# Performance work log

Hardware: AMD Instinct MI355X
Metric: run time of the kernel (lower is better)

The kernel has to match this reference:

```python
import jax, jax.numpy as jnp
import numpy as np

GRID_SIZE = 5
SPLINE_ORDER = 3
KH, KW = 3, 3
STRIDE, PAD, DIL = 1, 1, 1


def make_grid(in_features, dtype=jnp.float32):
    # uniform grid over [-1, 1], extended by spline_order on each side
    h = 2.0 / GRID_SIZE
    g = jnp.arange(-SPLINE_ORDER, GRID_SIZE + SPLINE_ORDER + 1, dtype=dtype) * h - 1.0
    return jnp.broadcast_to(g, (in_features, g.shape[0]))  # (in, G)


def b_splines(x, grid):
    # x: (N, in); grid: (in, G). Cox-de Boor recursion.
    xg = x[..., None]  # (N, in, 1)
    bases = ((xg >= grid[:, :-1]) & (xg < grid[:, 1:])).astype(x.dtype)  # (N, in, G-1)
    for k in range(1, SPLINE_ORDER + 1):
        left = (xg - grid[:, : -(k + 1)]) / (grid[:, k:-1] - grid[:, : -(k + 1)])
        right = (grid[:, k + 1:] - xg) / (grid[:, k + 1:] - grid[:, 1:-k])
        bases = left * bases[..., :-1] + right * bases[..., 1:]
    return bases  # (N, in, grid_size + spline_order)


def setup_inputs() -> dict:
    key = jax.random.key(0)
    k1, k2, k3, k4 = jax.random.split(key, 4)
    B, C, H, W = 4, 64, 64, 64
    out_ch = 128
    patch_dim = C * KH * KW  # 576
    nbasis = GRID_SIZE + SPLINE_ORDER  # 8
    x = jax.random.normal(k1, (B, C, H, W), dtype=jnp.float32)
    base_weight = jax.random.normal(k2, (out_ch, patch_dim), dtype=jnp.float32) * 0.05
    spline_weight = jax.random.normal(k3, (out_ch, patch_dim, nbasis), dtype=jnp.float32) * 0.05
    spline_scaler = jax.random.normal(k4, (out_ch, patch_dim), dtype=jnp.float32) * 0.1 + 1.0
    return {"x": x, "base_weight": base_weight, "spline_weight": spline_weight, "spline_scaler": spline_scaler}


def reference(x, base_weight, spline_weight, spline_scaler):
    B, C, H, W = x.shape
    out_ch, patch_dim = base_weight.shape
    # im2col: (B, C*KH*KW, Ho, Wo), feature dim ordered (C, kh, kw) like F.unfold
    patches = jax.lax.conv_general_dilated_patches(
        x, filter_shape=(KH, KW), window_strides=(STRIDE, STRIDE),
        padding=((PAD, PAD), (PAD, PAD)), rhs_dilation=(DIL, DIL),
        dimension_numbers=("NCHW", "OIHW", "NCHW"))
    Ho = (H + 2 * PAD - DIL * (KH - 1) - 1) // STRIDE + 1
    Wo = (W + 2 * PAD - DIL * (KW - 1) - 1) // STRIDE + 1
    L = Ho * Wo
    p = patches.reshape(B, patch_dim, L).transpose(0, 2, 1).reshape(B * L, patch_dim)  # (N, D)
    grid = make_grid(patch_dim, p.dtype)
    base_out = jax.nn.silu(p) @ base_weight.T  # (N, out)
    bases = b_splines(p, grid)  # (N, D, nbasis)
    scaled_w = spline_weight * spline_scaler[..., None]  # (out, D, nbasis)
    spline_out = jnp.einsum("ndk,odk->no", bases, scaled_w)
    out = (base_out + spline_out).reshape(B, L, out_ch).transpose(0, 2, 1).reshape(B, out_ch, Ho, Wo)
    return out
```

## Files before the change

kernel.cpp:

```cpp
#include <hip/hip_runtime.h>
#include <hip/hip_bf16.h>

#define B_      4
#define C_IN    64
#define H_      64
#define W_      64
#define OUT_CH  128
#define HP_     66
#define CF      576
#define WP_BYTES  (9 * OUT_CH * CF * 2)
#define F_BYTES   (B_ * HP_ * HP_ * CF * 2)
#define P_OFFSET  (WP_BYTES + F_BYTES)

typedef __bf16 bf16x8 __attribute__((ext_vector_type(8)));
typedef float  f32x4  __attribute__((ext_vector_type(4)));
typedef _Float16 half8 __attribute__((ext_vector_type(8)));

__device__ __forceinline__ void compute_features(float x, float f[9]) {
    f[0] = x / (1.0f + __expf(-x));
    float g[12];
#pragma unroll
    for (int i = 0; i < 12; ++i) g[i] = (float)(i - 3) * 0.4f - 1.0f;
    float bb[11];
#pragma unroll
    for (int i = 0; i < 11; ++i) bb[i] = (x >= g[i] && x < g[i + 1]) ? 1.0f : 0.0f;
#pragma unroll
    for (int i = 0; i < 10; ++i)
        bb[i] = (x - g[i]) * (1.0f / (g[i + 1] - g[i])) * bb[i]
              + (g[i + 2] - x) * (1.0f / (g[i + 2] - g[i + 1])) * bb[i + 1];
#pragma unroll
    for (int i = 0; i < 9; ++i)
        bb[i] = (x - g[i]) * (1.0f / (g[i + 2] - g[i])) * bb[i]
              + (g[i + 3] - x) * (1.0f / (g[i + 3] - g[i + 1])) * bb[i + 1];
#pragma unroll
    for (int i = 0; i < 8; ++i)
        bb[i] = (x - g[i]) * (1.0f / (g[i + 3] - g[i])) * bb[i]
              + (g[i + 4] - x) * (1.0f / (g[i + 4] - g[i + 1])) * bb[i + 1];
#pragma unroll
    for (int i = 0; i < 8; ++i) f[1 + i] = bb[i];
}

__global__ __launch_bounds__(256) void prep_kernel(
        const float* __restrict__ x, __hip_bfloat16* __restrict__ F,
        const float* __restrict__ bw, const float* __restrict__ sw,
        const float* __restrict__ sc, __hip_bfloat16* __restrict__ Wp) {
    __shared__ float xs[64][33];
    int blk = blockIdx.x;
    int tid = threadIdx.x;

    if (blk >= 528) {
        int idx = (blk - 528) * 256 + tid;
        if (idx < 589824) {
            int o = idx / 4608;
            int r = idx - o * 4608;
            int d = r >> 3;
            int j = r & 7;
            int tap = d % 9;
            int c   = d / 9;
            float v = sw[idx] * sc[o * 576 + d];
            Wp[(tap * OUT_CH + o) * CF + (j + 1) * 64 + c] = __float2bfloat16(v);
        } else {
            int k = idx - 589824;
            int o = k / 576;
            int d = k - o * 576;
            int tap = d % 9;
            int c   = d / 9;
            Wp[(tap * OUT_CH + o) * CF + c] = __float2bfloat16(bw[k]);
        }
        return;
    }

    int half = blk & 1;
    int bh   = blk >> 1;
    int b  = bh / HP_;
    int hp = bh % HP_;
    int h  = hp - 1;

    float f0[9];
    compute_features(0.0f, f0);

    bool interior_row = (h >= 0) && (h < H_);
    if (interior_row) {
        int wl = tid & 31;
        int c8 = tid >> 5;
#pragma unroll
        for (int i = 0; i < 8; ++i) {
            int c = c8 * 8 + i;
            xs[c][wl] = x[((b * C_IN + c) * H_ + h) * W_ + half * 32 + wl];
        }
    }
    __syncthreads();

    int c  = tid & 63;
    int wg = tid >> 6;
    __hip_bfloat16* Frow = F + (size_t)((b * HP_ + hp) * HP_) * CF;

    if (!interior_row) {
        for (int wp = half * 33 + wg; wp < half * 33 + 33; wp += 4) {
            __hip_bfloat16* dst = Frow + (size_t)wp * CF + c;
#pragma unroll
            for (int j = 0; j < 9; ++j) dst[j * 64] = __float2bfloat16(f0[j]);
        }
        return;
    }
    if (half == 0 && wg == 0) {
        __hip_bfloat16* dst = Frow + c;
#pragma unroll
        for (int j = 0; j < 9; ++j) dst[j * 64] = __float2bfloat16(f0[j]);
    }
    if (half == 1 && wg == 3) {
        __hip_bfloat16* dst = Frow + (size_t)65 * CF + c;
#pragma unroll
        for (int j = 0; j < 9; ++j) dst[j * 64] = __float2bfloat16(f0[j]);
    }
    for (int w2l = wg; w2l < 32; w2l += 4) {
        float xv = xs[c][w2l];
        float f[9];
        compute_features(xv, f);
        int wp = half * 32 + w2l + 1;
        __hip_bfloat16* dst = Frow + (size_t)wp * CF + c;
#pragma unroll
        for (int j = 0; j < 9; ++j) dst[j * 64] = __float2bfloat16(f[j]);
    }
}

__global__ __launch_bounds__(256, 2) void gemm_kernel(
        const __hip_bfloat16* __restrict__ Fb, const __hip_bfloat16* __restrict__ Wpb,
        _Float16* __restrict__ P) {
    __shared__ __align__(16) ushort As[2][8192];
    __shared__ __align__(16) ushort Bs[2][8192];

    const ushort* F  = (const ushort*)Fb;
    const ushort* Wp = (const ushort*)Wpb;

    int tid  = threadIdx.x;
    int lane = tid & 63;
    int w    = tid >> 6;
    int l15  = lane & 15;
    int lq   = lane >> 4;
    int wm = w & 1;
    int wn = w >> 1;
    int srow = lane >> 3;
    int sl7  = lane & 7;
    int c8s  = sl7 ^ srow;

    int blk = blockIdx.x;
    int g   = blk >> 7;
    int t   = blk & 127;
    int b   = t >> 5;
    int ho0 = (t & 31) << 1;
    int c0 = (g == 0) ? 0 : (21 + 20 * (g - 1));
    int c1 = c0 + ((g == 0) ? 21 : 20);

    f32x4 acc[4][4];
#pragma unroll
    for (int i = 0; i < 4; ++i)
#pragma unroll
        for (int j = 0; j < 4; ++j) acc[i][j] = (f32x4){0.f, 0.f, 0.f, 0.f};

    auto prefetch = [&](int ch, int buf) {
        int tap = ch / 9;
        int kc  = ch - tap * 9;
        int kh  = tap / 3;
        int kw  = tap - kh * 3;
#pragma unroll
        for (int r = 0; r < 4; ++r) {
            int row = (r * 4 + w) * 8 + srow;
            int hp = ho0 + (row >> 6) + kh;
            int wp = (row & 63) + kw;
            const ushort* srcA = F + (size_t)((b * HP_ + hp) * HP_ + wp) * CF
                                   + kc * 64 + c8s * 8;
            __builtin_amdgcn_global_load_lds(
                (const __attribute__((address_space(1))) unsigned int*)srcA,
                (__attribute__((address_space(3))) unsigned int*)&As[buf][(r * 4 + w) * 512],
                16, 0, 0);
            const ushort* srcB = Wp + (size_t)(tap * OUT_CH + row) * CF
                                    + kc * 64 + c8s * 8;
            __builtin_amdgcn_global_load_lds(
                (const __attribute__((address_space(1))) unsigned int*)srcB,
                (__attribute__((address_space(3))) unsigned int*)&Bs[buf][(r * 4 + w) * 512],
                16, 0, 0);
        }
    };

    int buf = 0;
    prefetch(c0, 0);
    prefetch(c0 + 1, 1);
    for (int ch = c0; ch < c1; ++ch) {
        if (ch + 1 < c1) asm volatile("s_waitcnt vmcnt(8)\n\ts_barrier" ::: "memory");
        else             asm volatile("s_waitcnt vmcnt(0)\n\ts_barrier" ::: "memory");

        bf16x8 af[2][4], bq[2][4];
#pragma unroll
        for (int ks = 0; ks < 2; ++ks) {
#pragma unroll
            for (int mt = 0; mt < 4; ++mt) {
                int o  = wm * 64 + mt * 16 + l15;
                int sl = o * 8 + ((ks * 4 + lq) ^ (o & 7));
                af[ks][mt] = *(const bf16x8*)&Bs[buf][sl * 8];
            }
#pragma unroll
            for (int nt = 0; nt < 4; ++nt) {
                int p  = wn * 64 + nt * 16 + l15;
                int sl = p * 8 + ((ks * 4 + lq) ^ (p & 7));
                bq[ks][nt] = *(const bf16x8*)&As[buf][sl * 8];
            }
        }
        asm volatile("s_waitcnt lgkmcnt(0)\n\ts_barrier" ::: "memory");
        if (ch + 2 < c1) prefetch(ch + 2, buf);

        __builtin_amdgcn_s_setprio(1);
#pragma unroll
        for (int ks = 0; ks < 2; ++ks)
#pragma unroll
            for (int mt = 0; mt < 4; ++mt)
#pragma unroll
                for (int nt = 0; nt < 4; ++nt)
                    acc[mt][nt] = __builtin_amdgcn_mfma_f32_16x16x32_bf16(
                        af[ks][mt], bq[ks][nt], acc[mt][nt], 0, 0, 0);
        __builtin_amdgcn_s_setprio(0);
        buf ^= 1;
    }

    _Float16* Pg = P + ((size_t)(g * 4 + b) * OUT_CH) * 4096 + ho0 * 64;
#pragma unroll
    for (int mt = 0; mt < 4; ++mt) {
        int o = wm * 64 + mt * 16 + lq * 4;
#pragma unroll
        for (int nt = 0; nt < 4; ++nt) {
            int pix = wn * 64 + nt * 16 + l15;
            _Float16* dst = Pg + (size_t)o * 4096 + pix;
#pragma unroll
            for (int r = 0; r < 4; ++r)
                dst[(size_t)r * 4096] = (_Float16)acc[mt][nt][r];
        }
    }
}

__global__ __launch_bounds__(256) void reduce_kernel(
        const half8* __restrict__ P, float4* __restrict__ out) {
    const int GS = 262144;
    int i = blockIdx.x * 256 + threadIdx.x;
    half8 a = P[i], bb = P[GS + i], c = P[2 * GS + i], d = P[3 * GS + i];
    float4 o0, o1;
#pragma unroll
    for (int j = 0; j < 4; ++j)
        ((float*)&o0)[j] = (float)a[j] + (float)bb[j] + (float)c[j] + (float)d[j];
#pragma unroll
    for (int j = 0; j < 4; ++j)
        ((float*)&o1)[j] = (float)a[4 + j] + (float)bb[4 + j] + (float)c[4 + j] + (float)d[4 + j];
    out[i * 2]     = o0;
    out[i * 2 + 1] = o1;
}

extern "C" void kernel_launch(void* const* d_in, const int* in_sizes, int n_in,
                              void* d_out, int out_size, void* d_ws, size_t ws_size,
                              hipStream_t stream) {
    const float* x  = (const float*)d_in[0];
    const float* bw = (const float*)d_in[1];
    const float* sw = (const float*)d_in[2];
    const float* sc = (const float*)d_in[3];
    float* out = (float*)d_out;

    __hip_bfloat16* Wp = (__hip_bfloat16*)d_ws;
    __hip_bfloat16* F  = (__hip_bfloat16*)((char*)d_ws + WP_BYTES);
    _Float16*       P  = (_Float16*)((char*)d_ws + P_OFFSET);

    prep_kernel<<<528 + 2592, 256, 0, stream>>>(x, F, bw, sw, sc, Wp);
    gemm_kernel<<<512, 256, 0, stream>>>(F, Wp, P);
    reduce_kernel<<<1024, 256, 0, stream>>>((const half8*)P, (float4*)out);
}
```

Baseline: 104.9 us.

## Pre-swizzle weights into MFMA fragment order and load directly to registers

The prep kernel now writes the combined base/spline weights in the exact per-lane MFMA fragment layout for each K-chunk. The GEMM then loads them straight from global memory into registers, double-buffered across iterations, instead of staging them through LDS. The freed LDS goes to a third activation buffer, giving a three-stage pipeline with vmcnt-based waits. This removes the weight LDS traffic and its bank pressure, at the cost of more VGPRs and global-load latency that must be hidden behind the MFMAs.

```diff
diff --git a/kernel.cpp b/kernel.cpp
--- a/kernel.cpp
+++ b/kernel.cpp
@@ -43,30 +43,29 @@
 __global__ __launch_bounds__(256) void prep_kernel(
         const float* __restrict__ x, __hip_bfloat16* __restrict__ F,
         const float* __restrict__ bw, const float* __restrict__ sw,
-        const float* __restrict__ sc, __hip_bfloat16* __restrict__ Wp) {
+        const float* __restrict__ sc, __hip_bfloat16* __restrict__ Wq) {
     __shared__ float xs[64][33];
     int blk = blockIdx.x;
     int tid = threadIdx.x;
 
     if (blk >= 528) {
         int idx = (blk - 528) * 256 + tid;
-        if (idx < 589824) {
-            int o = idx / 4608;
-            int r = idx - o * 4608;
-            int d = r >> 3;
-            int j = r & 7;
-            int tap = d % 9;
-            int c   = d / 9;
-            float v = sw[idx] * sc[o * 576 + d];
-            Wp[(tap * OUT_CH + o) * CF + (j + 1) * 64 + c] = __float2bfloat16(v);
-        } else {
-            int k = idx - 589824;
-            int o = k / 576;
-            int d = k - o * 576;
-            int tap = d % 9;
-            int c   = d / 9;
-            Wp[(tap * OUT_CH + o) * CF + c] = __float2bfloat16(bw[k]);
-        }
+        int e   = idx & 7;
+        int l15 = (idx >> 3) & 15;
+        int lq  = (idx >> 7) & 3;
+        int ks  = (idx >> 9) & 1;
+        int mt  = (idx >> 10) & 3;
+        int wm  = (idx >> 12) & 1;
+        int ch  = idx >> 13;
+        int kc  = ch % 9;
+        int tap = ch / 9;
+        int o   = wm * 64 + mt * 16 + l15;
+        int c   = (ks * 4 + lq) * 8 + e;
+        int d   = c * 9 + tap;
+        float v;
+        if (kc == 0) v = bw[o * 576 + d];
+        else         v = sw[(o * 576 + d) * 8 + (kc - 1)] * sc[o * 576 + d];
+        Wq[idx] = __float2bfloat16(v);
         return;
     }
 
@@ -125,13 +124,12 @@
 }
 
 __global__ __launch_bounds__(256, 2) void gemm_kernel(
-        const __hip_bfloat16* __restrict__ Fb, const __hip_bfloat16* __restrict__ Wpb,
+        const __hip_bfloat16* __restrict__ Fb, const __hip_bfloat16* __restrict__ Wqb,
         _Float16* __restrict__ P) {
-    __shared__ __align__(16) ushort As[2][8192];
-    __shared__ __align__(16) ushort Bs[2][8192];
+    __shared__ __align__(16) ushort As[3][8192];
 
     const ushort* F  = (const ushort*)Fb;
-    const ushort* Wp = (const ushort*)Wpb;
+    const ushort* Wq = (const ushort*)Wqb;
 
     int tid  = threadIdx.x;
     int lane = tid & 63;
@@ -150,7 +148,7 @@
     int b   = t >> 5;
     int ho0 = (t & 31) << 1;
     int c0 = (g == 0) ? 0 : (21 + 20 * (g - 1));
-    int c1 = c0 + ((g == 0) ? 21 : 20);
+    int nc = (g == 0) ? 21 : 20;
 
     f32x4 acc[4][4];
 #pragma unroll
@@ -158,7 +156,7 @@
 #pragma unroll
         for (int j = 0; j < 4; ++j) acc[i][j] = (f32x4){0.f, 0.f, 0.f, 0.f};
 
-    auto prefetch = [&](int ch, int buf) {
+    auto stage = [&](int ch, int bo) {
         int tap = ch / 9;
         int kc  = ch - tap * 9;
         int kh  = tap / 3;
@@ -172,55 +170,76 @@
                                    + kc * 64 + c8s * 8;
             __builtin_amdgcn_global_load_lds(
                 (const __attribute__((address_space(1))) unsigned int*)srcA,
-                (__attribute__((address_space(3))) unsigned int*)&As[buf][(r * 4 + w) * 512],
+                (__attribute__((address_space(3))) unsigned int*)&As[bo][(r * 4 + w) * 512],
                 16, 0, 0);
-            const ushort* srcB = Wp + (size_t)(tap * OUT_CH + row) * CF
-                                    + kc * 64 + c8s * 8;
-            __builtin_amdgcn_global_load_lds(
-                (const __attribute__((address_space(1))) unsigned int*)srcB,
-                (__attribute__((address_space(3))) unsigned int*)&Bs[buf][(r * 4 + w) * 512],
-                16, 0, 0);
         }
     };
 
-    int buf = 0;
-    prefetch(c0, 0);
-    prefetch(c0 + 1, 1);
-    for (int ch = c0; ch < c1; ++ch) {
-        if (ch + 1 < c1) asm volatile("s_waitcnt vmcnt(8)\n\ts_barrier" ::: "memory");
-        else             asm volatile("s_waitcnt vmcnt(0)\n\ts_barrier" ::: "memory");
-
-        bf16x8 af[2][4], bq[2][4];
-#pragma unroll
-        for (int ks = 0; ks < 2; ++ks) {
-#pragma unroll
-            for (int mt = 0; mt < 4; ++mt) {
-                int o  = wm * 64 + mt * 16 + l15;
-                int sl = o * 8 + ((ks * 4 + lq) ^ (o & 7));
-                af[ks][mt] = *(const bf16x8*)&Bs[buf][sl * 8];
-            }
-#pragma unroll
-            for (int nt = 0; nt < 4; ++nt) {
-                int p  = wn * 64 + nt * 16 + l15;
-                int sl = p * 8 + ((ks * 4 + lq) ^ (p & 7));
-                bq[ks][nt] = *(const bf16x8*)&As[buf][sl * 8];
-            }
-        }
-        asm volatile("s_waitcnt lgkmcnt(0)\n\ts_barrier" ::: "memory");
-        if (ch + 2 < c1) prefetch(ch + 2, buf);
-
-        __builtin_amdgcn_s_setprio(1);
-#pragma unroll
-        for (int ks = 0; ks < 2; ++ks)
-#pragma unroll
-            for (int mt = 0; mt < 4; ++mt)
-#pragma unroll
-                for (int nt = 0; nt < 4; ++nt)
-                    acc[mt][nt] = __builtin_amdgcn_mfma_f32_16x16x32_bf16(
-                        af[ks][mt], bq[ks][nt], acc[mt][nt], 0, 0, 0);
-        __builtin_amdgcn_s_setprio(0);
-        buf ^= 1;
-    }
+    bf16x8 afA[2][4], afB[2][4];
+
+#define LOAD_AF(AF, CH)                                                        \
+    {                                                                          \
+        const ushort* Wc = Wq + (size_t)(CH) * 8192;                           \
+        _Pragma("unroll")                                                      \
+        for (int ks = 0; ks < 2; ++ks)                                         \
+            _Pragma("unroll")                                                  \
+            for (int mt = 0; mt < 4; ++mt)                                     \
+                AF[ks][mt] = *(const bf16x8*)(Wc + ((wm * 4 + mt) * 2 + ks) * 512 \
+                                              + lane * 8);                     \
+    }
+
+#define GEMM_ITER(I, AFU, AFP)                                                 \
+    {                                                                          \
+        const int i_ = (I);                                                    \
+        asm volatile("s_barrier" ::: "memory");        \
+        if (i_ + 1 < nc) LOAD_AF(AFP, c0 + i_ + 1);    \
+        bf16x8 bq[2][4];                                                       \
+        _Pragma("unroll")                                                      \
+        for (int ks = 0; ks < 2; ++ks)                                         \
+            _Pragma("unroll")                                                  \
+            for (int nt = 0; nt < 4; ++nt) {                                   \
+                int p  = wn * 64 + nt * 16 + l15;                              \
+                int sl = p * 8 + ((ks * 4 + lq) ^ (p & 7));                    \
+                bq[ks][nt] = *(const bf16x8*)&As[bufo][sl * 8];                \
+            }                                                                  \
+        asm volatile("s_waitcnt lgkmcnt(0)\n\ts_barrier" ::: "memory");  \
+        if (i_ + 3 < nc) stage(c0 + i_ + 3, bufo);     \
+        {                                                                      \
+            int rem = nc - i_;                                                 \
+            if (rem > 3)       asm volatile("s_waitcnt vmcnt(16)" ::: "memory"); \
+            else if (rem == 3) asm volatile("s_waitcnt vmcnt(12)" ::: "memory"); \
+            else if (rem == 2) asm volatile("s_waitcnt vmcnt(8)"  ::: "memory"); \
+            else               asm volatile("s_waitcnt vmcnt(0)"  ::: "memory"); \
+        }                                                                      \
+        __builtin_amdgcn_s_setprio(1);                                         \
+        _Pragma("unroll")                                                      \
+        for (int ks = 0; ks < 2; ++ks)                                         \
+            _Pragma("unroll")                                                  \
+            for (int mt = 0; mt < 4; ++mt)                                     \
+                _Pragma("unroll")                                              \
+                for (int nt = 0; nt < 4; ++nt)                                 \
+                    acc[mt][nt] = __builtin_amdgcn_mfma_f32_16x16x32_bf16(     \
+                        AFU[ks][mt], bq[ks][nt], acc[mt][nt], 0, 0, 0);        \
+        __builtin_amdgcn_s_setprio(0);                                         \
+        bufo = (bufo == 2) ? 0 : bufo + 1;                                     \
+    }
+
+    LOAD_AF(afA, c0);
+    stage(c0 + 0, 0);
+    stage(c0 + 1, 1);
+    stage(c0 + 2, 2);
+    asm volatile("s_waitcnt vmcnt(8)" ::: "memory");
+
+    int bufo = 0;
+    int i = 0;
+    for (; i + 1 < nc; i += 2) {
+        GEMM_ITER(i, afA, afB);
+        GEMM_ITER(i + 1, afB, afA);
+    }
+    if (i < nc) GEMM_ITER(i, afA, afB);
+
+#undef GEMM_ITER
+#undef LOAD_AF
 
     _Float16* Pg = P + ((size_t)(g * 4 + b) * OUT_CH) * 4096 + ho0 * 64;
 #pragma unroll
@@ -262,11 +281,11 @@
     const float* sc = (const float*)d_in[3];
     float* out = (float*)d_out;
 
-    __hip_bfloat16* Wp = (__hip_bfloat16*)d_ws;
+    __hip_bfloat16* Wq = (__hip_bfloat16*)d_ws;
     __hip_bfloat16* F  = (__hip_bfloat16*)((char*)d_ws + WP_BYTES);
     _Float16*       P  = (_Float16*)((char*)d_ws + P_OFFSET);
 
-    prep_kernel<<<528 + 2592, 256, 0, stream>>>(x, F, bw, sw, sc, Wp);
-    gemm_kernel<<<512, 256, 0, stream>>>(F, Wp, P);
+    prep_kernel<<<528 + 2592, 256, 0, stream>>>(x, F, bw, sw, sc, Wq);
+    gemm_kernel<<<512, 256, 0, stream>>>(F, Wq, P);
     reduce_kernel<<<1024, 256, 0, stream>>>((const half8*)P, (float4*)out);
 }
```

Measured after the change: 107.0 us. About the same (+1.9%).

## Replace split-K partial buffer and reduce kernel with atomic adds into output

Applied to the files above, without the earlier changes.

The separate reduce kernel and the fp16 partial buffer are removed. The output is now zeroed by extra blocks in the prep kernel, and each GEMM block atomically adds its fp32 accumulators straight into the output. The block index is also remapped so the four K-split groups for the same tile are spread across blocks, probably across XCDs, to reduce atomic contention. This saves one kernel launch and the round trip through the partial buffer, but adds atomic traffic, and the summation order of the splits is no longer fixed.

```diff
diff --git a/kernel.cpp b/kernel.cpp
--- a/kernel.cpp
+++ b/kernel.cpp
@@ -10,11 +10,9 @@
 #define CF      576
 #define WP_BYTES  (9 * OUT_CH * CF * 2)
 #define F_BYTES   (B_ * HP_ * HP_ * CF * 2)
-#define P_OFFSET  (WP_BYTES + F_BYTES)
 
 typedef __bf16 bf16x8 __attribute__((ext_vector_type(8)));
 typedef float  f32x4  __attribute__((ext_vector_type(4)));
-typedef _Float16 half8 __attribute__((ext_vector_type(8)));
 
 __device__ __forceinline__ void compute_features(float x, float f[9]) {
     f[0] = x / (1.0f + __expf(-x));
@@ -43,10 +41,20 @@
 __global__ __launch_bounds__(256) void prep_kernel(
         const float* __restrict__ x, __hip_bfloat16* __restrict__ F,
         const float* __restrict__ bw, const float* __restrict__ sw,
-        const float* __restrict__ sc, __hip_bfloat16* __restrict__ Wp) {
+        const float* __restrict__ sc, __hip_bfloat16* __restrict__ Wp,
+        float* __restrict__ out) {
     __shared__ float xs[64][33];
     int blk = blockIdx.x;
     int tid = threadIdx.x;
+
+    if (blk >= 3120) {
+        int zb = blk - 3120;
+        float4* dst = (float4*)out + (size_t)zb * 1024 + tid;
+        float4 z = make_float4(0.f, 0.f, 0.f, 0.f);
+#pragma unroll
+        for (int k = 0; k < 4; ++k) dst[k * 256] = z;
+        return;
+    }
 
     if (blk >= 528) {
         int idx = (blk - 528) * 256 + tid;
@@ -126,7 +134,7 @@
 
 __global__ __launch_bounds__(256, 2) void gemm_kernel(
         const __hip_bfloat16* __restrict__ Fb, const __hip_bfloat16* __restrict__ Wpb,
-        _Float16* __restrict__ P) {
+        float* __restrict__ out) {
     __shared__ __align__(16) ushort As[2][8192];
     __shared__ __align__(16) ushort Bs[2][8192];
 
@@ -144,11 +152,13 @@
     int sl7  = lane & 7;
     int c8s  = sl7 ^ srow;
 
-    int blk = blockIdx.x;
-    int g   = blk >> 7;
-    int t   = blk & 127;
-    int b   = t >> 5;
-    int ho0 = (t & 31) << 1;
+    int hwb = blockIdx.x;
+    int l   = ((hwb & 7) << 6) | (hwb >> 3);
+    int q   = l >> 6;
+    int r   = l & 63;
+    int b   = q >> 1;
+    int g   = ((q & 1) << 1) | (r >> 5);
+    int ho0 = (r & 31) << 1;
     int c0 = (g == 0) ? 0 : (21 + 20 * (g - 1));
     int c1 = c0 + ((g == 0) ? 21 : 20);
 
@@ -164,21 +174,21 @@
         int kh  = tap / 3;
         int kw  = tap - kh * 3;
 #pragma unroll
-        for (int r = 0; r < 4; ++r) {
-            int row = (r * 4 + w) * 8 + srow;
+        for (int rr = 0; rr < 4; ++rr) {
+            int row = (rr * 4 + w) * 8 + srow;
             int hp = ho0 + (row >> 6) + kh;
             int wp = (row & 63) + kw;
             const ushort* srcA = F + (size_t)((b * HP_ + hp) * HP_ + wp) * CF
                                    + kc * 64 + c8s * 8;
             __builtin_amdgcn_global_load_lds(
                 (const __attribute__((address_space(1))) unsigned int*)srcA,
-                (__attribute__((address_space(3))) unsigned int*)&As[buf][(r * 4 + w) * 512],
+                (__attribute__((address_space(3))) unsigned int*)&As[buf][(rr * 4 + w) * 512],
                 16, 0, 0);
             const ushort* srcB = Wp + (size_t)(tap * OUT_CH + row) * CF
                                     + kc * 64 + c8s * 8;
             __builtin_amdgcn_global_load_lds(
                 (const __attribute__((address_space(1))) unsigned int*)srcB,
-                (__attribute__((address_space(3))) unsigned int*)&Bs[buf][(r * 4 + w) * 512],
+                (__attribute__((address_space(3))) unsigned int*)&Bs[buf][(rr * 4 + w) * 512],
                 16, 0, 0);
         }
     };
@@ -222,35 +232,19 @@
         buf ^= 1;
     }
 
-    _Float16* Pg = P + ((size_t)(g * 4 + b) * OUT_CH) * 4096 + ho0 * 64;
+    float* Og = out + ((size_t)b * OUT_CH) * 4096 + ho0 * 64;
 #pragma unroll
     for (int mt = 0; mt < 4; ++mt) {
         int o = wm * 64 + mt * 16 + lq * 4;
 #pragma unroll
         for (int nt = 0; nt < 4; ++nt) {
             int pix = wn * 64 + nt * 16 + l15;
-            _Float16* dst = Pg + (size_t)o * 4096 + pix;
-#pragma unroll
-            for (int r = 0; r < 4; ++r)
-                dst[(size_t)r * 4096] = (_Float16)acc[mt][nt][r];
-        }
-    }
-}
-
-__global__ __launch_bounds__(256) void reduce_kernel(
-        const half8* __restrict__ P, float4* __restrict__ out) {
-    const int GS = 262144;
-    int i = blockIdx.x * 256 + threadIdx.x;
-    half8 a = P[i], bb = P[GS + i], c = P[2 * GS + i], d = P[3 * GS + i];
-    float4 o0, o1;
-#pragma unroll
-    for (int j = 0; j < 4; ++j)
-        ((float*)&o0)[j] = (float)a[j] + (float)bb[j] + (float)c[j] + (float)d[j];
-#pragma unroll
-    for (int j = 0; j < 4; ++j)
-        ((float*)&o1)[j] = (float)a[4 + j] + (float)bb[4 + j] + (float)c[4 + j] + (float)d[4 + j];
-    out[i * 2]     = o0;
-    out[i * 2 + 1] = o1;
+            float* dst = Og + (size_t)o * 4096 + pix;
+#pragma unroll
+            for (int rr = 0; rr < 4; ++rr)
+                unsafeAtomicAdd(dst + (size_t)rr * 4096, acc[mt][nt][rr]);
+        }
+    }
 }
 
 extern "C" void kernel_launch(void* const* d_in, const int* in_sizes, int n_in,
@@ -264,9 +258,7 @@
 
     __hip_bfloat16* Wp = (__hip_bfloat16*)d_ws;
     __hip_bfloat16* F  = (__hip_bfloat16*)((char*)d_ws + WP_BYTES);
-    _Float16*       P  = (_Float16*)((char*)d_ws + P_OFFSET);
-
-    prep_kernel<<<528 + 2592, 256, 0, stream>>>(x, F, bw, sw, sc, Wp);
-    gemm_kernel<<<512, 256, 0, stream>>>(F, Wp, P);
-    reduce_kernel<<<1024, 256, 0, stream>>>((const half8*)P, (float4*)out);
-}
+
+    prep_kernel<<<3632, 256, 0, stream>>>(x, F, bw, sw, sc, Wp, out);
+    gemm_kernel<<<512, 256, 0, stream>>>(F, Wp, out);
+}
```

New measurement: 125.9 us. 19.9% more time.
